# Optimization experiments

Hardware: AMD Instinct MI355X
Metric: run time of the kernel (lower is better)

The kernel has to match this reference:

```python
import jax, jax.numpy as jnp
import numpy as np

HID = 4096
NH = 32
NKV = 8
HD = 128
KV_OUT = NKV * HD  # 1024
B, S = 1, 2048
SCALE = 64.0
THETA = 500000.0


def fwht(x):
    """Normalized fast Walsh-Hadamard transform over last dim (power of 2).
    Matches matmul_hadU_cuda for the had=None, K=1 case."""
    *lead, n = x.shape
    x = x.reshape(-1, n)
    h = 1
    while h < n:  # log2(n) static iterations
        x = x.reshape(-1, n // (2 * h), 2, h)
        a, b = x[:, :, 0, :], x[:, :, 1, :]
        x = jnp.stack([a + b, a - b], axis=2).reshape(-1, n)
        h *= 2
    return (x * (1.0 / np.sqrt(n))).reshape(*lead, n)


def rope_cos_sin(position_ids, dim=HD, theta=THETA):
    inv_freq = 1.0 / (theta ** (jnp.arange(0, dim, 2, dtype=jnp.float32) / dim))
    freqs = position_ids.astype(jnp.float32)[..., None] * inv_freq  # [B,S,HD/2]
    emb = jnp.concatenate([freqs, freqs], axis=-1)  # [B,S,HD]
    return jnp.cos(emb), jnp.sin(emb)


def rotate_half(x):
    h = x.shape[-1] // 2
    return jnp.concatenate([-x[..., h:], x[..., :h]], axis=-1)


def setup_inputs() -> dict:
    key = jax.random.key(0)
    ks = jax.random.split(key, 10)
    return {
        "hidden_states": jax.random.normal(ks[0], (B, S, HID), jnp.float32),
        "position_ids": jnp.arange(S, dtype=jnp.int32)[None, :],
        "SU_qkv": jnp.sign(jax.random.normal(ks[1], (HID,), jnp.float32)),
        "SU_o": jnp.sign(jax.random.normal(ks[2], (HID,), jnp.float32)),
        "Wscale_qkv": jax.random.uniform(ks[3], (HID + 2 * KV_OUT,), jnp.float32, 0.5, 1.5),
        "Wscale_o": jax.random.uniform(ks[4], (HID,), jnp.float32, 0.5, 1.5),
        "Wq": 0.02 * jax.random.normal(ks[5], (HID, HID), jnp.float32),
        "Wk": 0.02 * jax.random.normal(ks[6], (KV_OUT, HID), jnp.float32),
        "Wv": 0.02 * jax.random.normal(ks[7], (KV_OUT, HID), jnp.float32),
        "Wo": 0.02 * jax.random.normal(ks[8], (HID, HID), jnp.float32),
    }


def reference(hidden_states, position_ids, SU_qkv, SU_o, Wscale_qkv, Wscale_o, Wq, Wk, Wv, Wo):
    b, s, n = hidden_states.shape
    # --- compute_qkv: incoherence rotation + quantized-linear math ---
    x = fwht(hidden_states * SU_qkv) / SCALE  # [B,S,HID]
    q = (x @ Wq.T) * Wscale_qkv[:HID] * SCALE
    k = (x @ Wk.T) * Wscale_qkv[HID:HID + KV_OUT] * SCALE
    v = (x @ Wv.T) * Wscale_qkv[HID + KV_OUT:] * SCALE
    q = q.reshape(b, s, NH, HD).transpose(0, 2, 1, 3)   # [B,NH,S,HD]
    k = k.reshape(b, s, NKV, HD).transpose(0, 2, 1, 3)  # [B,NKV,S,HD]
    v = v.reshape(b, s, NKV, HD).transpose(0, 2, 1, 3)
    # --- RoPE ---
    cos, sin = rope_cos_sin(position_ids)
    cos, sin = cos[:, None], sin[:, None]  # [B,1,S,HD]
    q = q * cos + rotate_half(q) * sin
    k = k * cos + rotate_half(k) * sin
    # --- GQA repeat + causal SDPA ---
    rep = NH // NKV
    k = jnp.repeat(k, rep, axis=1)
    v = jnp.repeat(v, rep, axis=1)
    scores = jnp.einsum('bhqd,bhkd->bhqk', q, k) / np.sqrt(HD)
    causal = jnp.tril(jnp.ones((s, s), dtype=bool))
    scores = jnp.where(causal, scores, -1e30)
    attn = jax.nn.softmax(scores, axis=-1)
    out = jnp.einsum('bhqk,bhkd->bhqd', attn, v)
    out = out.transpose(0, 2, 1, 3).reshape(b, s, NH * HD)  # [B,S,HID]
    # --- compute_o ---
    y = fwht(out * SU_o) / SCALE
    y = (y @ Wo.T) * Wscale_o * SCALE
    return y
```

## Files before the change

### kernel.cpp

```cpp
#include <hip/hip_runtime.h>
#include <hip/hip_bf16.h>
#include <math.h>

#define S_LEN 2048
#define HID   4096
#define NQKV  6144
#define NHEAD 32
#define NKVH  8
#define HDIM  128

typedef __attribute__((ext_vector_type(8))) short short8;
typedef __attribute__((ext_vector_type(4))) float f32x4;

__device__ __forceinline__ unsigned short f2bf(float f) {
    union { float f; unsigned u; } v; v.f = f;
    unsigned r = v.u + 0x7fffu + ((v.u >> 16) & 1u);
    return (unsigned short)(r >> 16);
}
__device__ __forceinline__ float bf2f(unsigned short b) {
    union { unsigned u; float f; } v; v.u = ((unsigned)b) << 16;
    return v.f;
}
__device__ __forceinline__ unsigned cvt_pk_bf16(float lo, float hi) {
    unsigned r;
    asm("v_cvt_pk_bf16_f32 %0, %1, %2" : "=v"(r) : "v"(lo), "v"(hi));
    return r;
}

__global__ __launch_bounds__(256)
void cvt4_kernel(const float* __restrict__ Wq, const float* __restrict__ Wk,
                 const float* __restrict__ Wv, const float* __restrict__ Wo,
                 unsigned short* __restrict__ Wcat, unsigned short* __restrict__ Wob) {
    const int NQ = 4194304, NK = 1048576, NV = 1048576, NO = 4194304;
    int i = blockIdx.x * 256 + threadIdx.x;
    const int stride = gridDim.x * 256;
    for (; i < NQ + NK + NV + NO; i += stride) {
        const float* src; unsigned short* dst; int j;
        if (i < NQ)                { src = Wq; dst = Wcat;            j = i; }
        else if (i < NQ + NK)      { src = Wk; dst = Wcat + 16777216; j = i - NQ; }
        else if (i < NQ + NK + NV) { src = Wv; dst = Wcat + 20971520; j = i - NQ - NK; }
        else                       { src = Wo; dst = Wob;             j = i - NQ - NK - NV; }
        float4 v = *(const float4*)(src + (size_t)j * 4);
        ushort4 o;
        o.x = f2bf(v.x); o.y = f2bf(v.y); o.z = f2bf(v.z); o.w = f2bf(v.w);
        *(ushort4*)(dst + (size_t)j * 4) = o;
    }
}

__global__ __launch_bounds__(256)
void fwht_kernel(const float* __restrict__ in, const float* __restrict__ su,
                 unsigned short* __restrict__ out) {
    __shared__ float buf[HID];
    const float* src = in + (size_t)blockIdx.x * HID;
    for (int i = threadIdx.x; i < HID; i += 256) buf[i] = src[i] * su[i];
    __syncthreads();
    int lg = 0;
    for (int h = 1; h < HID; h <<= 1, ++lg) {
        for (int p = threadIdx.x; p < HID / 2; p += 256) {
            int j  = p & (h - 1);
            int i0 = ((p >> lg) << (lg + 1)) | j;
            int i1 = i0 + h;
            float a = buf[i0], b = buf[i1];
            buf[i0] = a + b;
            buf[i1] = a - b;
        }
        __syncthreads();
    }
    unsigned short* dst = out + (size_t)blockIdx.x * HID;
    const float norm = 1.0f / 4096.0f;
    for (int i = threadIdx.x; i < HID; i += 256) dst[i] = f2bf(buf[i] * norm);
}

__global__ __launch_bounds__(256)
void fwht_merge(const unsigned short* __restrict__ O1, const float* __restrict__ ML,
                const float* __restrict__ su, unsigned short* __restrict__ out) {
    __shared__ float buf[HID];
    __shared__ float w1s[NHEAD], w2s[NHEAD], w3s[NHEAD];
    const int q = blockIdx.x;
    if (threadIdx.x < NHEAD) {
        const float2* mlp = (const float2*)ML;
        float2 a = mlp[((size_t)q) * NHEAD + threadIdx.x];
        float2 b = mlp[((size_t)(S_LEN + q)) * NHEAD + threadIdx.x];
        float2 c = mlp[((size_t)(2 * S_LEN + q)) * NHEAD + threadIdx.x];
        float M = fmaxf(fmaxf(a.x, b.x), c.x);
        float e1 = exp2f(a.x - M), e2 = exp2f(b.x - M), e3 = exp2f(c.x - M);
        float L = e1 * a.y + e2 * b.y + e3 * c.y;
        w1s[threadIdx.x] = e1 / L;
        w2s[threadIdx.x] = e2 / L;
        w3s[threadIdx.x] = e3 / L;
    }
    __syncthreads();
    const unsigned short* r1 = O1 + (size_t)q * HID;
    const unsigned short* r2 = O1 + (size_t)(S_LEN + q) * HID;
    const unsigned short* r3 = O1 + (size_t)(2 * S_LEN + q) * HID;
    for (int i = threadIdx.x; i < HID; i += 256) {
        int hd = i >> 7;
        buf[i] = (bf2f(r1[i]) * w1s[hd] + bf2f(r2[i]) * w2s[hd] + bf2f(r3[i]) * w3s[hd]) * su[i];
    }
    __syncthreads();
    int lg = 0;
    for (int h = 1; h < HID; h <<= 1, ++lg) {
        for (int p = threadIdx.x; p < HID / 2; p += 256) {
            int j  = p & (h - 1);
            int i0 = ((p >> lg) << (lg + 1)) | j;
            int i1 = i0 + h;
            float a = buf[i0], b = buf[i1];
            buf[i0] = a + b;
            buf[i1] = a - b;
        }
        __syncthreads();
    }
    unsigned short* dst = out + (size_t)q * HID;
    const float norm = 1.0f / 4096.0f;
    for (int i = threadIdx.x; i < HID; i += 256) dst[i] = f2bf(buf[i] * norm);
}

__global__ __launch_bounds__(256)
void gemm_bt(const unsigned short* __restrict__ A, const unsigned short* __restrict__ B,
             const float* __restrict__ scale, float* __restrict__ C,
             int M, int N, int K) {
    __shared__ __attribute__((aligned(16))) unsigned short As[2][128 * 32];
    __shared__ __attribute__((aligned(16))) unsigned short Bs[2][128 * 32];
    const int bn = blockIdx.x, bm = blockIdx.y;
    const int tid = threadIdx.x;
    const int wv = tid >> 6, lane = tid & 63;
    const int wr = wv >> 1, wc = wv & 1;
    const int lr = lane & 15, lgp = lane >> 4;

    f32x4 acc[4][4] = {};

    auto stage = [&](int buf, int kt) {
        for (int c = wv; c < 8; c += 4) {
            int o = c * 512 + lane * 8;
            int row = o >> 5, col = o & 31;
            const unsigned short* ga = A + (size_t)(bm * 128 + row) * K + kt * 32 + col;
            __builtin_amdgcn_global_load_lds((const __attribute__((address_space(1))) void*)ga,
                (__attribute__((address_space(3))) void*)&As[buf][c * 512], 16, 0, 0);
            const unsigned short* gb = B + (size_t)(bn * 128 + row) * K + kt * 32 + col;
            __builtin_amdgcn_global_load_lds((const __attribute__((address_space(1))) void*)gb,
                (__attribute__((address_space(3))) void*)&Bs[buf][c * 512], 16, 0, 0);
        }
    };

    const int nt = K >> 5;
    stage(0, 0);
    __syncthreads();
    int cur = 0;
    for (int kt = 0; kt < nt; ++kt) {
        if (kt + 1 < nt) stage(cur ^ 1, kt + 1);
        const int ko = lgp * 8;
        short8 af[4], bfr[4];
#pragma unroll
        for (int m2 = 0; m2 < 4; ++m2)
            af[m2] = *(const short8*)&As[cur][(wr * 64 + m2 * 16 + lr) * 32 + ko];
#pragma unroll
        for (int n2 = 0; n2 < 4; ++n2)
            bfr[n2] = *(const short8*)&Bs[cur][(wc * 64 + n2 * 16 + lr) * 32 + ko];
#pragma unroll
        for (int m2 = 0; m2 < 4; ++m2)
#pragma unroll
            for (int n2 = 0; n2 < 4; ++n2)
                acc[m2][n2] = __builtin_amdgcn_mfma_f32_16x16x32_bf16(af[m2], bfr[n2], acc[m2][n2], 0, 0, 0);
        __syncthreads();
        cur ^= 1;
    }

#pragma unroll
    for (int n2 = 0; n2 < 4; ++n2) {
        int gn = bn * 128 + wc * 64 + n2 * 16 + lr;
        float sc = scale[gn] * 64.0f;
#pragma unroll
        for (int m2 = 0; m2 < 4; ++m2) {
            int gm0 = bm * 128 + wr * 64 + m2 * 16 + lgp * 4;
#pragma unroll
            for (int i = 0; i < 4; ++i)
                C[(size_t)(gm0 + i) * N + gn] = acc[m2][n2][i] * sc;
        }
    }
}

__global__ __launch_bounds__(256)
void gemm_qkv(const unsigned short* __restrict__ A, const unsigned short* __restrict__ B,
              const float* __restrict__ scale, const int* __restrict__ pos,
              unsigned short* __restrict__ Qb, unsigned short* __restrict__ Kb,
              unsigned short* __restrict__ Vb) {
    const int K = HID;
    __shared__ __attribute__((aligned(16))) unsigned short As[2][128 * 32];
    __shared__ __attribute__((aligned(16))) unsigned short Bs[2][128 * 32];
    __shared__ float invf_t[64];
    __shared__ float poss[128];
    const int bn = blockIdx.x, bm = blockIdx.y;
    const int tid = threadIdx.x;
    const int wv = tid >> 6, lane = tid & 63;
    const int wr = wv >> 1, wc = wv & 1;
    const int lr = lane & 15, lgp = lane >> 4;

    if (tid < 64) invf_t[tid] = exp2f((float)tid * -0.29580576f);
    if (tid >= 128) poss[tid - 128] = (float)pos[bm * 128 + (tid - 128)];

    f32x4 acc[4][4] = {};

    auto stage = [&](int buf, int kt) {
        for (int c = wv; c < 8; c += 4) {
            int o = c * 512 + lane * 8;
            int row = o >> 5, col = o & 31;
            const unsigned short* ga = A + (size_t)(bm * 128 + row) * K + kt * 32 + col;
            __builtin_amdgcn_global_load_lds((const __attribute__((address_space(1))) void*)ga,
                (__attribute__((address_space(3))) void*)&As[buf][c * 512], 16, 0, 0);
            int prow = (row & 31) | ((row & 32) << 1) | ((row & 64) >> 1);
            const unsigned short* gb = B + (size_t)(bn * 128 + prow) * K + kt * 32 + col;
            __builtin_amdgcn_global_load_lds((const __attribute__((address_space(1))) void*)gb,
                (__attribute__((address_space(3))) void*)&Bs[buf][c * 512], 16, 0, 0);
        }
    };

    const int nt = K >> 5;
    stage(0, 0);
    __syncthreads();
    int cur = 0;
    for (int kt = 0; kt < nt; ++kt) {
        if (kt + 1 < nt) stage(cur ^ 1, kt + 1);
        const int ko = lgp * 8;
        short8 af[4], bfr[4];
#pragma unroll
        for (int m2 = 0; m2 < 4; ++m2)
            af[m2] = *(const short8*)&As[cur][(wr * 64 + m2 * 16 + lr) * 32 + ko];
#pragma unroll
        for (int n2 = 0; n2 < 4; ++n2)
            bfr[n2] = *(const short8*)&Bs[cur][(wc * 64 + n2 * 16 + lr) * 32 + ko];
#pragma unroll
        for (int m2 = 0; m2 < 4; ++m2)
#pragma unroll
            for (int n2 = 0; n2 < 4; ++n2)
                acc[m2][n2] = __builtin_amdgcn_mfma_f32_16x16x32_bf16(af[m2], bfr[n2], acc[m2][n2], 0, 0, 0);
        __syncthreads();
        cur ^= 1;
    }

    const int nb = bn * 128;
    const float QS = 0.12751793f;
#pragma unroll
    for (int n2 = 0; n2 < 2; ++n2) {
        const int d = n2 * 16 + lr + wc * 32;
        const float sc_lo = scale[nb + d] * 64.0f;
        const float sc_hi = scale[nb + d + 64] * 64.0f;
        const float ivf = invf_t[d];
#pragma unroll
        for (int m2 = 0; m2 < 4; ++m2) {
#pragma unroll
            for (int i = 0; i < 4; ++i) {
                const int lrow = wr * 64 + m2 * 16 + lgp * 4 + i;
                const int srow = bm * 128 + lrow;
                float lo = acc[m2][n2][i] * sc_lo;
                float hi = acc[m2][n2 + 2][i] * sc_hi;
                float olo, ohi;
                if (bn < 40) {
                    float sn, cs;
                    sincosf(poss[lrow] * ivf, &sn, &cs);
                    olo = lo * cs - hi * sn;
                    ohi = hi * cs + lo * sn;
                } else { olo = lo; ohi = hi; }
                unsigned short* dst;
                if (bn < 32)      { dst = Qb + ((size_t)bn * S_LEN + srow) * HDIM; olo *= QS; ohi *= QS; }
                else if (bn < 40) { dst = Kb + ((size_t)(bn - 32) * S_LEN + srow) * HDIM; }
                else              { dst = Vb + ((size_t)(bn - 40) * S_LEN + srow) * HDIM; }
                dst[d]      = f2bf(olo);
                dst[d + 64] = f2bf(ohi);
            }
        }
    }
}

__global__ __launch_bounds__(256)
void attn_kernel(const unsigned short* __restrict__ Q, const unsigned short* __restrict__ K,
                 const unsigned short* __restrict__ V, unsigned short* __restrict__ Opart,
                 float* __restrict__ ML) {
    const int hf = blockIdx.y;
    const int hd = blockIdx.z;
    const int kvh = hd >> 2;
    const int tid = threadIdx.x, wv = tid >> 6, lane = tid & 63;
    const int lr = lane & 15, lgp = lane >> 4;

    __shared__ __attribute__((aligned(16))) unsigned short Ks[2][64 * 128];
    __shared__ __attribute__((aligned(16))) unsigned short Vt[128 * 64];

    int koff[4];
#pragma unroll
    for (int j = 0; j < 4; ++j) {
        int a = (wv * 4 + j) * 512 + lane * 8;
        koff[j] = a ^ (((a >> 7) & 7) << 3);
    }
    const int vpos = ((lane >> 2) & 3) * 16 + (lane >> 4) * 4 + (lane & 3);
    const unsigned short* Kg = K + (size_t)kvh * S_LEN * HDIM;
    const unsigned short* Vg = V + (size_t)kvh * S_LEN * HDIM;

    auto stageK = [&](int buf, int kb) {
        const unsigned short* kg = Kg + (size_t)kb * 64 * HDIM;
#pragma unroll
        for (int j = 0; j < 4; ++j) {
            __builtin_amdgcn_global_load_lds(
                (const __attribute__((address_space(1))) void*)(kg + koff[j]),
                (__attribute__((address_space(3))) void*)&Ks[buf][(wv * 4 + j) * 512], 16, 0, 0);
        }
    };

#pragma unroll 1
    for (int rep = 0; rep < 2; ++rep) {
        const int qt = rep ? (31 - (int)blockIdx.x) : (int)blockIdx.x;
        const int qg = qt * 64 + wv * 16 + lr;
        const int n = qt + 1;
        const int s = (n * hf) / 3, e = (n * (hf + 1)) / 3;

        __syncthreads();

        short8 aq[4];
        {
            const unsigned short* qp = Q + ((size_t)hd * S_LEN + qg) * HDIM + lgp * 8;
#pragma unroll
            for (int kk = 0; kk < 4; ++kk) aq[kk] = *(const short8*)(qp + kk * 32);
        }

        f32x4 oacc[8] = {};
        float m_i = -3.0e38f, l_i = 0.f;

        short8 vcur[4];
        if (s < e) {
            stageK(s & 1, s);
            const unsigned short* vp = Vg + (size_t)s * 64 * HDIM + lane * HDIM + wv * 32;
#pragma unroll
            for (int r2 = 0; r2 < 4; ++r2) vcur[r2] = *(const short8*)(vp + r2 * 8);
        }

#pragma unroll 1
        for (int kb = s; kb < e; ++kb) {
            const int cur = kb & 1;
            __syncthreads();

            if (kb + 1 < e) stageK(cur ^ 1, kb + 1);
#pragma unroll
            for (int r2 = 0; r2 < 4; ++r2) {
#pragma unroll
                for (int en = 0; en < 8; ++en) {
                    int d = wv * 32 + r2 * 8 + en;
                    Vt[(d * 64 + vpos) ^ ((d & 7) << 3)] = ((const unsigned short*)&vcur[r2])[en];
                }
            }
            if (kb + 1 < e) {
                const unsigned short* vp = Vg + (size_t)(kb + 1) * 64 * HDIM + lane * HDIM + wv * 32;
#pragma unroll
                for (int r2 = 0; r2 < 4; ++r2) vcur[r2] = *(const short8*)(vp + r2 * 8);
            }

            __builtin_amdgcn_s_setprio(1);
            f32x4 sc[4];
#pragma unroll
            for (int nt2 = 0; nt2 < 4; ++nt2) {
                f32x4 a = {};
                const int krow = nt2 * 16 + lr;
                const int swz = (krow & 7) << 3;
#pragma unroll
                for (int kk = 0; kk < 4; ++kk) {
                    short8 ak = *(const short8*)&Ks[cur][(krow * 128 + kk * 32 + lgp * 8) ^ swz];
                    a = __builtin_amdgcn_mfma_f32_16x16x32_bf16(ak, aq[kk], a, 0, 0, 0);
                }
                sc[nt2] = a;
            }
            __builtin_amdgcn_s_setprio(0);

            if (kb == qt) {
#pragma unroll
                for (int nt2 = 0; nt2 < 4; ++nt2)
#pragma unroll
                    for (int i = 0; i < 4; ++i) {
                        int kvg = kb * 64 + nt2 * 16 + 4 * lgp + i;
                        if (kvg > qg) sc[nt2][i] = -1.0e30f;
                    }
            }

            float vmax = fmaxf(fmaxf(fmaxf(sc[0][0], sc[0][1]), fmaxf(sc[0][2], sc[0][3])),
                               fmaxf(fmaxf(sc[1][0], sc[1][1]), fmaxf(sc[1][2], sc[1][3])));
            vmax = fmaxf(vmax, fmaxf(fmaxf(fmaxf(sc[2][0], sc[2][1]), fmaxf(sc[2][2], sc[2][3])),
                                     fmaxf(fmaxf(sc[3][0], sc[3][1]), fmaxf(sc[3][2], sc[3][3]))));
            vmax = fmaxf(vmax, __shfl_xor(vmax, 16));
            vmax = fmaxf(vmax, __shfl_xor(vmax, 32));

            if (!__all(vmax <= m_i + 11.0f)) {
                float mn = fmaxf(m_i, vmax);
                float fe = __builtin_amdgcn_exp2f(m_i - mn);
                m_i = mn;
                l_i *= fe;
                float feb[4];
#pragma unroll
                for (int i2 = 0; i2 < 4; ++i2) feb[i2] = __shfl(fe, 4 * lgp + i2);
#pragma unroll
                for (int t = 0; t < 8; ++t)
#pragma unroll
                    for (int i2 = 0; i2 < 4; ++i2) oacc[t][i2] *= feb[i2];
            }

            float rs = 0.f;
#pragma unroll
            for (int nt2 = 0; nt2 < 4; ++nt2)
#pragma unroll
                for (int i = 0; i < 4; ++i) {
                    float pv = __builtin_amdgcn_exp2f(sc[nt2][i] - m_i);
                    sc[nt2][i] = pv;
                    rs += pv;
                }
            rs += __shfl_xor(rs, 16);
            rs += __shfl_xor(rs, 32);
            l_i += rs;

            union { unsigned u[4]; short8 sv; } a0, a1;
            a0.u[0] = cvt_pk_bf16(sc[0][0], sc[0][1]);
            a0.u[1] = cvt_pk_bf16(sc[0][2], sc[0][3]);
            a0.u[2] = cvt_pk_bf16(sc[1][0], sc[1][1]);
            a0.u[3] = cvt_pk_bf16(sc[1][2], sc[1][3]);
            a1.u[0] = cvt_pk_bf16(sc[2][0], sc[2][1]);
            a1.u[1] = cvt_pk_bf16(sc[2][2], sc[2][3]);
            a1.u[2] = cvt_pk_bf16(sc[3][0], sc[3][1]);
            a1.u[3] = cvt_pk_bf16(sc[3][2], sc[3][3]);

            asm volatile("s_waitcnt lgkmcnt(0)" ::: "memory");
            __builtin_amdgcn_sched_barrier(0);
            __builtin_amdgcn_s_barrier();

            __builtin_amdgcn_s_setprio(1);
#pragma unroll
            for (int t = 0; t < 8; ++t) {
                const int d = t * 16 + lr;
                const int swz = (d & 7) << 3;
                const int dbase = d * 64 + lgp * 16;
                short8 bv0 = *(const short8*)&Vt[(dbase) ^ swz];
                short8 bv1 = *(const short8*)&Vt[(dbase + 8) ^ swz];
                oacc[t] = __builtin_amdgcn_mfma_f32_16x16x32_bf16(a0.sv, bv0, oacc[t], 0, 0, 0);
                oacc[t] = __builtin_amdgcn_mfma_f32_16x16x32_bf16(a1.sv, bv1, oacc[t], 0, 0, 0);
            }
            __builtin_amdgcn_s_setprio(0);
        }

        unsigned short* op = Opart + ((size_t)hf * S_LEN + qt * 64 + wv * 16 + 4 * lgp) * HID
                           + hd * HDIM + lr;
#pragma unroll
        for (int t = 0; t < 8; ++t)
#pragma unroll
            for (int i2 = 0; i2 < 4; ++i2)
                op[(size_t)i2 * HID + t * 16] = f2bf(oacc[t][i2]);
        if (lgp == 0) {
            float2* mlp = (float2*)ML;
            mlp[((size_t)hf * S_LEN + qt * 64 + wv * 16 + lr) * NHEAD + hd] =
                make_float2(m_i, l_i);
        }
    }
}

extern "C" void kernel_launch(void* const* d_in, const int* in_sizes, int n_in,
                              void* d_out, int out_size, void* d_ws, size_t ws_size,
                              hipStream_t stream) {
    const float* hidden = (const float*)d_in[0];
    const int*   pos    = (const int*)d_in[1];
    const float* su_qkv = (const float*)d_in[2];
    const float* su_o   = (const float*)d_in[3];
    const float* ws_qkv = (const float*)d_in[4];
    const float* ws_o   = (const float*)d_in[5];
    const float* Wq     = (const float*)d_in[6];
    const float* Wk     = (const float*)d_in[7];
    const float* Wv     = (const float*)d_in[8];
    const float* Wo     = (const float*)d_in[9];
    float* out = (float*)d_out;

    char* ws = (char*)d_ws;
    unsigned short* Wcat = (unsigned short*)(ws);
    unsigned short* Wob  = (unsigned short*)(ws + 50331648);
    unsigned short* xb   = (unsigned short*)(ws + 83886080);
    unsigned short* Opart= (unsigned short*)(ws + 100663296);
    float*          ML   = (float*)(ws);
    unsigned short* Qb   = (unsigned short*)(ws + 150994944);
    unsigned short* Kb   = Qb + (size_t)NHEAD * S_LEN * HDIM;
    unsigned short* Vb   = Kb + (size_t)NKVH * S_LEN * HDIM;

    cvt4_kernel<<<2560, 256, 0, stream>>>(Wq, Wk, Wv, Wo, Wcat, Wob);

    fwht_kernel<<<S_LEN, 256, 0, stream>>>(hidden, su_qkv, xb);
    gemm_qkv<<<dim3(NQKV / 128, S_LEN / 128), 256, 0, stream>>>(xb, Wcat, ws_qkv, pos, Qb, Kb, Vb);
    attn_kernel<<<dim3(16, 3, NHEAD), 256, 0, stream>>>(Qb, Kb, Vb, Opart, ML);
    fwht_merge<<<S_LEN, 256, 0, stream>>>(Opart, ML, su_o, xb);
    gemm_bt<<<dim3(HID / 128, S_LEN / 128), 256, 0, stream>>>(xb, Wob, ws_o, out, S_LEN, HID, HID);
}
```

Measured before the change: 442.1 us.

## Use radix-4 FWHT stages and split attention KV range in two instead of three

Replaces the radix-2 shared-memory Walsh-Hadamard butterfly with a radix-4 version, halving the number of passes and barriers in both FWHT kernels. The attention split-K factor drops from three partitions to two, so the merge kernel reads and combines two partial outputs instead of three, and the ML buffer moves to a separate workspace offset. Fewer partitions cut merge traffic and grid size but give fewer blocks per head for load balancing.

```diff
diff --git a/kernel.cpp b/kernel.cpp
--- a/kernel.cpp
+++ b/kernel.cpp
@@ -25,6 +25,23 @@
     unsigned r;
     asm("v_cvt_pk_bf16_f32 %0, %1, %2" : "=v"(r) : "v"(lo), "v"(hi));
     return r;
+}
+
+__device__ __forceinline__ void fwht_lds_radix4(float* buf) {
+    int lg = 0;
+    for (int h = 1; h < HID; h <<= 2, lg += 2) {
+        for (int p = threadIdx.x; p < HID / 4; p += 256) {
+            int j  = p & (h - 1);
+            int i0 = ((p >> lg) << (lg + 2)) | j;
+            float a = buf[i0], b = buf[i0 + h], c = buf[i0 + 2 * h], d = buf[i0 + 3 * h];
+            float apb = a + b, amb = a - b, cpd = c + d, cmd = c - d;
+            buf[i0]         = apb + cpd;
+            buf[i0 + h]     = amb + cmd;
+            buf[i0 + 2 * h] = apb - cpd;
+            buf[i0 + 3 * h] = amb - cmd;
+        }
+        __syncthreads();
+    }
 }
 
 __global__ __launch_bounds__(256)
@@ -54,18 +71,7 @@
     const float* src = in + (size_t)blockIdx.x * HID;
     for (int i = threadIdx.x; i < HID; i += 256) buf[i] = src[i] * su[i];
     __syncthreads();
-    int lg = 0;
-    for (int h = 1; h < HID; h <<= 1, ++lg) {
-        for (int p = threadIdx.x; p < HID / 2; p += 256) {
-            int j  = p & (h - 1);
-            int i0 = ((p >> lg) << (lg + 1)) | j;
-            int i1 = i0 + h;
-            float a = buf[i0], b = buf[i1];
-            buf[i0] = a + b;
-            buf[i1] = a - b;
-        }
-        __syncthreads();
-    }
+    fwht_lds_radix4(buf);
     unsigned short* dst = out + (size_t)blockIdx.x * HID;
     const float norm = 1.0f / 4096.0f;
     for (int i = threadIdx.x; i < HID; i += 256) dst[i] = f2bf(buf[i] * norm);
@@ -75,41 +81,27 @@
 void fwht_merge(const unsigned short* __restrict__ O1, const float* __restrict__ ML,
                 const float* __restrict__ su, unsigned short* __restrict__ out) {
     __shared__ float buf[HID];
-    __shared__ float w1s[NHEAD], w2s[NHEAD], w3s[NHEAD];
+    __shared__ float w1s[NHEAD], w2s[NHEAD];
     const int q = blockIdx.x;
     if (threadIdx.x < NHEAD) {
         const float2* mlp = (const float2*)ML;
         float2 a = mlp[((size_t)q) * NHEAD + threadIdx.x];
         float2 b = mlp[((size_t)(S_LEN + q)) * NHEAD + threadIdx.x];
-        float2 c = mlp[((size_t)(2 * S_LEN + q)) * NHEAD + threadIdx.x];
-        float M = fmaxf(fmaxf(a.x, b.x), c.x);
-        float e1 = exp2f(a.x - M), e2 = exp2f(b.x - M), e3 = exp2f(c.x - M);
-        float L = e1 * a.y + e2 * b.y + e3 * c.y;
+        float M = fmaxf(a.x, b.x);
+        float e1 = exp2f(a.x - M), e2 = exp2f(b.x - M);
+        float L = e1 * a.y + e2 * b.y;
         w1s[threadIdx.x] = e1 / L;
         w2s[threadIdx.x] = e2 / L;
-        w3s[threadIdx.x] = e3 / L;
     }
     __syncthreads();
     const unsigned short* r1 = O1 + (size_t)q * HID;
     const unsigned short* r2 = O1 + (size_t)(S_LEN + q) * HID;
-    const unsigned short* r3 = O1 + (size_t)(2 * S_LEN + q) * HID;
     for (int i = threadIdx.x; i < HID; i += 256) {
         int hd = i >> 7;
-        buf[i] = (bf2f(r1[i]) * w1s[hd] + bf2f(r2[i]) * w2s[hd] + bf2f(r3[i]) * w3s[hd]) * su[i];
+        buf[i] = (bf2f(r1[i]) * w1s[hd] + bf2f(r2[i]) * w2s[hd]) * su[i];
     }
     __syncthreads();
-    int lg = 0;
-    for (int h = 1; h < HID; h <<= 1, ++lg) {
-        for (int p = threadIdx.x; p < HID / 2; p += 256) {
-            int j  = p & (h - 1);
-            int i0 = ((p >> lg) << (lg + 1)) | j;
-            int i1 = i0 + h;
-            float a = buf[i0], b = buf[i1];
-            buf[i0] = a + b;
-            buf[i1] = a - b;
-        }
-        __syncthreads();
-    }
+    fwht_lds_radix4(buf);
     unsigned short* dst = out + (size_t)q * HID;
     const float norm = 1.0f / 4096.0f;
     for (int i = threadIdx.x; i < HID; i += 256) dst[i] = f2bf(buf[i] * norm);
@@ -308,8 +300,8 @@
     for (int rep = 0; rep < 2; ++rep) {
         const int qt = rep ? (31 - (int)blockIdx.x) : (int)blockIdx.x;
         const int qg = qt * 64 + wv * 16 + lr;
-        const int n = qt + 1;
-        const int s = (n * hf) / 3, e = (n * (hf + 1)) / 3;
+        const int n = qt + 1, mid = (n + 1) >> 1;
+        const int s = hf ? mid : 0, e = hf ? n : mid;
 
         __syncthreads();
 
@@ -474,7 +466,7 @@
     unsigned short* Wob  = (unsigned short*)(ws + 50331648);
     unsigned short* xb   = (unsigned short*)(ws + 83886080);
     unsigned short* Opart= (unsigned short*)(ws + 100663296);
-    float*          ML   = (float*)(ws);
+    float*          ML   = (float*)(ws + 100663296 + 33554432);
     unsigned short* Qb   = (unsigned short*)(ws + 150994944);
     unsigned short* Kb   = Qb + (size_t)NHEAD * S_LEN * HDIM;
     unsigned short* Vb   = Kb + (size_t)NKVH * S_LEN * HDIM;
@@ -483,7 +475,7 @@
 
     fwht_kernel<<<S_LEN, 256, 0, stream>>>(hidden, su_qkv, xb);
     gemm_qkv<<<dim3(NQKV / 128, S_LEN / 128), 256, 0, stream>>>(xb, Wcat, ws_qkv, pos, Qb, Kb, Vb);
-    attn_kernel<<<dim3(16, 3, NHEAD), 256, 0, stream>>>(Qb, Kb, Vb, Opart, ML);
+    attn_kernel<<<dim3(16, 2, NHEAD), 256, 0, stream>>>(Qb, Kb, Vb, Opart, ML);
     fwht_merge<<<S_LEN, 256, 0, stream>>>(Opart, ML, su_o, xb);
     gemm_bt<<<dim3(HID / 128, S_LEN / 128), 256, 0, stream>>>(xb, Wob, ws_o, out, S_LEN, HID, HID);
 }
```

After: 409.9 us. -7.3%, faster.
